# Performance work log

Measured on AMD Instinct MI355X. Metric: run time of the kernel, lower is better.

## Reference

```python
import jax, jax.numpy as jnp
import numpy as np

INPUT_SIZE = 768
HIDDEN = 512


def _lstm_dir(x_tbi, h0, c0, w_ih, w_hh, b_ih, b_hh):
    """Single-direction LSTM over time-major input. Returns all hidden states [T,B,H].
    PyTorch gate order: i, f, g, o."""
    # Precompute input contribution for all timesteps (one big GEMM).
    gx = jnp.einsum('tbi,gi->tbg', x_tbi, w_ih) + (b_ih + b_hh)  # [T,B,4H]

    def step(carry, gx_t):
        h, c = carry
        gates = gx_t + h @ w_hh.T  # [B,4H]
        i, f, g, o = jnp.split(gates, 4, axis=-1)
        i = jax.nn.sigmoid(i)
        f = jax.nn.sigmoid(f)
        g = jnp.tanh(g)
        o = jax.nn.sigmoid(o)
        c = f * c + i * g
        h = o * jnp.tanh(c)
        return (h, c), h

    (_, _), hs = jax.lax.scan(step, (h0, c0), gx)
    return hs  # [T,B,H]


def setup_inputs() -> dict:
    key = jax.random.key(0)
    ks = jax.random.split(key, 12)
    B, T = 32, 512
    scale = 1.0 / np.sqrt(HIDDEN)

    def unif(k, shape):
        return jax.random.uniform(k, shape, jnp.float32, -scale, scale)

    return {
        'x': jax.random.normal(ks[0], (B, T, INPUT_SIZE), jnp.float32),
        'h0': jax.random.normal(ks[1], (2, B, HIDDEN), jnp.float32),
        'c0': jax.random.normal(ks[2], (2, B, HIDDEN), jnp.float32),
        'w_ih_f': unif(ks[3], (4 * HIDDEN, INPUT_SIZE)),
        'w_hh_f': unif(ks[4], (4 * HIDDEN, HIDDEN)),
        'b_ih_f': unif(ks[5], (4 * HIDDEN,)),
        'b_hh_f': unif(ks[6], (4 * HIDDEN,)),
        'w_ih_b': unif(ks[7], (4 * HIDDEN, INPUT_SIZE)),
        'w_hh_b': unif(ks[8], (4 * HIDDEN, HIDDEN)),
        'b_ih_b': unif(ks[9], (4 * HIDDEN,)),
        'b_hh_b': unif(ks[10], (4 * HIDDEN,)),
    }


def reference(x, h0, c0, w_ih_f, w_hh_f, b_ih_f, b_hh_f,
              w_ih_b, w_hh_b, b_ih_b, b_hh_b):
    # x: [B,T,I] (batch_first) -> time-major [T,B,I]
    x_tbi = jnp.transpose(x, (1, 0, 2))
    hs_f = _lstm_dir(x_tbi, h0[0], c0[0], w_ih_f, w_hh_f, b_ih_f, b_hh_f)
    hs_b = _lstm_dir(x_tbi[::-1], h0[1], c0[1], w_ih_b, w_hh_b, b_ih_b, b_hh_b)
    # out[:, -1, :]: forward dir at last step = hs_f[-1];
    # backward dir at last time index = first scan step over reversed seq = hs_b[0]
    last = jnp.concatenate([hs_f[-1], hs_b[0]], axis=-1)  # [B, 2H]
    return jax.nn.relu(last)
```

## Files before the change

kernel.cpp:

```cpp
#include <hip/hip_runtime.h>


typedef __attribute__((ext_vector_type(4))) float         floatx4;
typedef __attribute__((ext_vector_type(4))) unsigned int  uintx4;
typedef __attribute__((ext_vector_type(8))) unsigned short ushortx8;
typedef __attribute__((ext_vector_type(4))) unsigned short ushortx4;
typedef __attribute__((ext_vector_type(8))) __bf16        bf16x8;

#define NBLK 32
#define GRID_TOTAL 256
#define DONE_MAGIC 0xDEADBEEFu

__device__ __forceinline__ unsigned short f2bf(float f) {
  unsigned u = __builtin_bit_cast(unsigned, f);
  return (unsigned short)((u + 0x7fffu + ((u >> 16) & 1u)) >> 16);
}
__device__ __forceinline__ float bf2f(unsigned short h) {
  unsigned u = ((unsigned)h) << 16;
  return __builtin_bit_cast(float, u);
}
__device__ __forceinline__ floatx4 mfma_bf16(ushortx8 a, ushortx8 b, floatx4 c) {
  return __builtin_amdgcn_mfma_f32_16x16x32_bf16(
      __builtin_bit_cast(bf16x8, a), __builtin_bit_cast(bf16x8, b), c, 0, 0, 0);
}
__device__ __forceinline__ float sigmoidf_(float x) { return 1.f / (1.f + __expf(-x)); }
__device__ __forceinline__ float tanhf_(float x) {
  float ax = fabsf(x);
  float e = __expf(-2.f * ax);
  float r = (1.f - e) / (1.f + e);
  return x < 0.f ? -r : r;
}

__global__ void cvt_w_kernel(const float* __restrict__ src, unsigned short* __restrict__ dst, int n) {
  int i = (blockIdx.x * 256 + threadIdx.x) * 4;
  if (i < n) {
    floatx4 v = *reinterpret_cast<const floatx4*>(src + i);
    ushortx4 o;
    o[0] = f2bf(v[0]); o[1] = f2bf(v[1]); o[2] = f2bf(v[2]); o[3] = f2bf(v[3]);
    *reinterpret_cast<ushortx4*>(dst + i) = o;
  }
}

__global__ __launch_bounds__(256) void gx_kernel(
    const float* __restrict__ x, const unsigned short* __restrict__ w_bf,
    const float* __restrict__ b_ih, const float* __restrict__ b_hh,
    unsigned short* __restrict__ gxbuf) {
  const int t = blockIdx.y;
  const int nb = blockIdx.x;
  const int tid = threadIdx.x;
  const int wave = tid >> 6;
  const int lane = tid & 63;
  const int l15 = lane & 15;
  const int lq = lane >> 4;

  __shared__ __align__(16) unsigned short x_lds[32][776];

  {
    const int row = tid >> 3, c8 = tid & 7;
    const floatx4* src = reinterpret_cast<const floatx4*>(x + ((size_t)row * 512 + t) * 768);
#pragma unroll
    for (int m = 0; m < 24; ++m) {
      int col4 = c8 + m * 8;
      floatx4 v = src[col4];
      ushortx4 o;
      o[0] = f2bf(v[0]); o[1] = f2bf(v[1]); o[2] = f2bf(v[2]); o[3] = f2bf(v[3]);
      *reinterpret_cast<ushortx4*>(&x_lds[row][col4 * 4]) = o;
    }
  }
  __syncthreads();

  const int wgs = nb * 4;
  const ushortx8* brow[4];
#pragma unroll
  for (int nt = 0; nt < 4; ++nt) {
    int n = wave * 512 + (wgs + nt) * 16 + l15;
    brow[nt] = reinterpret_cast<const ushortx8*>(w_bf + (size_t)n * 768);
  }

  floatx4 acc[4][2];
#pragma unroll
  for (int nt = 0; nt < 4; ++nt) { acc[nt][0] = (floatx4)0.f; acc[nt][1] = (floatx4)0.f; }

  for (int q = 0; q < 24; ++q) {
    ushortx8 a0 = *reinterpret_cast<const ushortx8*>(&x_lds[l15][q * 32 + lq * 8]);
    ushortx8 a1 = *reinterpret_cast<const ushortx8*>(&x_lds[16 + l15][q * 32 + lq * 8]);
#pragma unroll
    for (int nt = 0; nt < 4; ++nt) {
      ushortx8 bf = brow[nt][q * 4 + lq];
      acc[nt][0] = mfma_bf16(a0, bf, acc[nt][0]);
      acc[nt][1] = mfma_bf16(a1, bf, acc[nt][1]);
    }
  }

#pragma unroll
  for (int nt = 0; nt < 4; ++nt) {
    int wg = wgs + nt;
    int N = wave * 512 + wg * 16 + l15;
    float bias = b_ih[N] + b_hh[N];
    unsigned short* dst = gxbuf + ((size_t)(t * 32 + wg)) * 2048 + wave * 512 + l15;
#pragma unroll
    for (int m = 0; m < 2; ++m)
#pragma unroll
      for (int r = 0; r < 4; ++r) {
        int b = m * 16 + lq * 4 + r;
        dst[b * 16] = f2bf(acc[nt][m][r] + bias);
      }
  }
}

__global__ __launch_bounds__(256) void bwd_kernel(
    const float* __restrict__ x, const float* __restrict__ h0, const float* __restrict__ c0,
    const float* __restrict__ w_ih_b, const float* __restrict__ w_hh_b,
    const float* __restrict__ b_ih_b, const float* __restrict__ b_hh_b,
    float* __restrict__ out) {
  const int wg = blockIdx.x;
  const int tid = threadIdx.x;
  const int wave = tid >> 6;
  const int lane = tid & 63;
  const int l15 = lane & 15;
  const int lq = lane >> 4;

  __shared__ __align__(16) unsigned short cat_lds[32][1288];
  __shared__ __align__(16) float gate_lds[4][32][16];

  {
    const int row = tid >> 3, o8 = tid & 7;
    const floatx4* xs = reinterpret_cast<const floatx4*>(x + ((size_t)row * 512 + 511) * 768);
#pragma unroll
    for (int m = 0; m < 24; ++m) {
      int col4 = o8 + m * 8;
      floatx4 v = xs[col4];
      ushortx4 o;
      o[0] = f2bf(v[0]); o[1] = f2bf(v[1]); o[2] = f2bf(v[2]); o[3] = f2bf(v[3]);
      *reinterpret_cast<ushortx4*>(&cat_lds[row][col4 * 4]) = o;
    }
    const floatx4* hs = reinterpret_cast<const floatx4*>(h0 + (size_t)(32 + row) * 512);
#pragma unroll
    for (int m = 0; m < 16; ++m) {
      int col4 = o8 + m * 8;
      floatx4 v = hs[col4];
      ushortx4 o;
      o[0] = f2bf(v[0]); o[1] = f2bf(v[1]); o[2] = f2bf(v[2]); o[3] = f2bf(v[3]);
      *reinterpret_cast<ushortx4*>(&cat_lds[row][768 + col4 * 4]) = o;
    }
  }
  __syncthreads();

  const int n = wave * 512 + wg * 16 + l15;
  floatx4 acc0 = (floatx4)0.f, acc1 = (floatx4)0.f;
  for (int q = 0; q < 40; ++q) {
    int k0 = q * 32;
    const float* wsrc = (k0 < 768) ? (w_ih_b + (size_t)n * 768 + k0 + lq * 8)
                                   : (w_hh_b + (size_t)n * 512 + (k0 - 768) + lq * 8);
    ushortx8 bf;
#pragma unroll
    for (int j = 0; j < 8; ++j) bf[j] = f2bf(wsrc[j]);
    ushortx8 a0 = *reinterpret_cast<const ushortx8*>(&cat_lds[l15][k0 + lq * 8]);
    ushortx8 a1 = *reinterpret_cast<const ushortx8*>(&cat_lds[16 + l15][k0 + lq * 8]);
    acc0 = mfma_bf16(a0, bf, acc0);
    acc1 = mfma_bf16(a1, bf, acc1);
  }
#pragma unroll
  for (int r = 0; r < 4; ++r) {
    gate_lds[wave][lq * 4 + r][l15] = acc0[r];
    gate_lds[wave][16 + lq * 4 + r][l15] = acc1[r];
  }
  __syncthreads();

  {
    const int jj = tid & 15;
    const int b0 = tid >> 4;
    const int col = wg * 16 + jj;
    float bi[4];
#pragma unroll
    for (int g = 0; g < 4; ++g) bi[g] = b_ih_b[g * 512 + col] + b_hh_b[g * 512 + col];
#pragma unroll
    for (int half = 0; half < 2; ++half) {
      int b = b0 + half * 16;
      float gi = sigmoidf_(gate_lds[0][b][jj] + bi[0]);
      float gf = sigmoidf_(gate_lds[1][b][jj] + bi[1]);
      float gg = tanhf_(gate_lds[2][b][jj] + bi[2]);
      float go = sigmoidf_(gate_lds[3][b][jj] + bi[3]);
      float c = gf * c0[(size_t)(32 + b) * 512 + col] + gi * gg;
      float h = go * tanhf_(c);
      out[(size_t)b * 1024 + 512 + col] = fmaxf(h, 0.f);
    }
  }
}

__global__ __launch_bounds__(256, 1) void lstm_fwd_kernel(
    const float* __restrict__ w_hh, const unsigned short* __restrict__ gxbuf,
    const float* __restrict__ h0, const float* __restrict__ c0,
    unsigned long long* gbuf64, unsigned* flags, float* sink,
    float* __restrict__ out) {
  const int tid = threadIdx.x;

  if ((blockIdx.x & 7) != 0) {
    __shared__ unsigned sdone;
    float a0 = 1.0f + 1e-7f * (float)(tid + 1);
    float a1 = 1.0f - 1e-7f * (float)(tid + 2);
    float a2 = 1.0f + 2e-7f * (float)(tid + 3);
    float a3 = 1.0f - 2e-7f * (float)(tid + 4);
    const float m0 = 0.99999994f;
    unsigned d;
    do {
#pragma unroll 8
      for (int i = 0; i < 2048; ++i) {
        a0 = fmaf(a0, m0, 1e-7f);
        a1 = fmaf(a1, m0, -1e-7f);
        a2 = fmaf(a2, m0, 2e-7f);
        a3 = fmaf(a3, m0, -2e-7f);
      }
      if (tid == 0)
        sdone = __hip_atomic_load(&flags[0], __ATOMIC_RELAXED, __HIP_MEMORY_SCOPE_AGENT);
      __syncthreads();
      d = sdone;
      __syncthreads();
    } while (d != DONE_MAGIC);
    if (a0 + a1 + a2 + a3 == 3.14159f) sink[blockIdx.x] = a0;
    return;
  }

  const int wg = blockIdx.x >> 3;
  const int wave = tid >> 6;
  const int lane = tid & 63;
  const int l15 = lane & 15;
  const int lq = lane >> 4;

  __shared__ __align__(16) unsigned short h_lds[32][520];
  __shared__ __align__(16) float gate_lds[4][32][16];
  __shared__ __align__(16) unsigned short gx_lds[2][2048];

  ushortx8 wfrag[16];
  {
    const int n = wave * 512 + wg * 16 + l15;
    const float* wrow = w_hh + (size_t)n * 512 + lq * 8;
#pragma unroll
    for (int q = 0; q < 16; ++q) {
      ushortx8 f;
#pragma unroll
      for (int j = 0; j < 8; ++j) f[j] = f2bf(wrow[q * 32 + j]);
      wfrag[q] = f;
    }
  }

  const int b_ = tid >> 3;
  const int j0 = (tid & 7) * 2;
  const int col0 = wg * 16 + j0;
  float c_0 = c0[(size_t)b_ * 512 + col0];
  float c_1 = c0[(size_t)b_ * 512 + col0 + 1];

  {
    unsigned data = (unsigned)f2bf(h0[(size_t)b_ * 512 + col0]) |
                    ((unsigned)f2bf(h0[(size_t)b_ * 512 + col0 + 1]) << 16);
    unsigned long long w = ((unsigned long long)data << 32) | 1ull;
    __hip_atomic_store(&gbuf64[b_ * 256 + (col0 >> 1)], w, __ATOMIC_RELAXED, __HIP_MEMORY_SCOPE_AGENT);
  }

  const uintx4* gxp = reinterpret_cast<const uintx4*>(gxbuf);
  uintx4 gxreg = gxp[(size_t)(0 * 32 + wg) * 256 + tid];

#pragma unroll 1
  for (int t = 0; t < 512; ++t) {
    *reinterpret_cast<uintx4*>(&gx_lds[t & 1][tid * 8]) = gxreg;
    if (t + 1 < 512) gxreg = gxp[(size_t)((t + 1) * 32 + wg) * 256 + tid];

    {
      unsigned long long* src = gbuf64 + (size_t)(t & 1) * 8192;
      const unsigned target = (unsigned)(t + 1);
      unsigned long long w[32];
      bool ok;
      do {
#pragma unroll
        for (int k = 0; k < 32; ++k)
          w[k] = __hip_atomic_load(&src[tid + k * 256], __ATOMIC_RELAXED, __HIP_MEMORY_SCOPE_AGENT);
        ok = true;
#pragma unroll
        for (int k = 0; k < 32; ++k) ok &= ((unsigned)w[k] == target);
      } while (!ok);
#pragma unroll
      for (int k = 0; k < 32; ++k)
        *reinterpret_cast<unsigned*>(&h_lds[k][tid * 2]) = (unsigned)(w[k] >> 32);
    }
    __syncthreads();

    floatx4 acc0 = (floatx4)0.f, acc1 = (floatx4)0.f;
#pragma unroll
    for (int q = 0; q < 16; ++q) {
      ushortx8 a0 = *reinterpret_cast<const ushortx8*>(&h_lds[l15][q * 32 + lq * 8]);
      ushortx8 a1 = *reinterpret_cast<const ushortx8*>(&h_lds[16 + l15][q * 32 + lq * 8]);
      acc0 = mfma_bf16(a0, wfrag[q], acc0);
      acc1 = mfma_bf16(a1, wfrag[q], acc1);
    }
#pragma unroll
    for (int r = 0; r < 4; ++r) {
      gate_lds[wave][lq * 4 + r][l15] = acc0[r];
      gate_lds[wave][16 + lq * 4 + r][l15] = acc1[r];
    }
    __syncthreads();

    {
      const unsigned short* gx = gx_lds[t & 1];
      float i0 = sigmoidf_(gate_lds[0][b_][j0] + bf2f(gx[(0 * 32 + b_) * 16 + j0]));
      float f0 = sigmoidf_(gate_lds[1][b_][j0] + bf2f(gx[(1 * 32 + b_) * 16 + j0]));
      float g0 = tanhf_(gate_lds[2][b_][j0] + bf2f(gx[(2 * 32 + b_) * 16 + j0]));
      float o0 = sigmoidf_(gate_lds[3][b_][j0] + bf2f(gx[(3 * 32 + b_) * 16 + j0]));
      c_0 = f0 * c_0 + i0 * g0;
      float ha = o0 * tanhf_(c_0);

      float i1 = sigmoidf_(gate_lds[0][b_][j0 + 1] + bf2f(gx[(0 * 32 + b_) * 16 + j0 + 1]));
      float f1 = sigmoidf_(gate_lds[1][b_][j0 + 1] + bf2f(gx[(1 * 32 + b_) * 16 + j0 + 1]));
      float g1 = tanhf_(gate_lds[2][b_][j0 + 1] + bf2f(gx[(2 * 32 + b_) * 16 + j0 + 1]));
      float o1 = sigmoidf_(gate_lds[3][b_][j0 + 1] + bf2f(gx[(3 * 32 + b_) * 16 + j0 + 1]));
      c_1 = f1 * c_1 + i1 * g1;
      float hb = o1 * tanhf_(c_1);

      unsigned data = (unsigned)f2bf(ha) | ((unsigned)f2bf(hb) << 16);
      unsigned long long w = ((unsigned long long)data << 32) | (unsigned long long)(t + 2);
      unsigned long long* hdst = gbuf64 + (size_t)((t + 1) & 1) * 8192;
      __hip_atomic_store(&hdst[b_ * 256 + (col0 >> 1)], w, __ATOMIC_RELAXED, __HIP_MEMORY_SCOPE_AGENT);
      if (t == 511) {
        out[(size_t)b_ * 1024 + col0] = fmaxf(ha, 0.f);
        out[(size_t)b_ * 1024 + col0 + 1] = fmaxf(hb, 0.f);
      }
    }
  }

  if (wg == 0 && tid == 0)
    __hip_atomic_store(&flags[0], DONE_MAGIC, __ATOMIC_RELAXED, __HIP_MEMORY_SCOPE_AGENT);
}

extern "C" void kernel_launch(void* const* d_in, const int* in_sizes, int n_in,
                              void* d_out, int out_size, void* d_ws, size_t ws_size,
                              hipStream_t stream) {
  const float* x      = (const float*)d_in[0];
  const float* h0     = (const float*)d_in[1];
  const float* c0     = (const float*)d_in[2];
  const float* w_ih_f = (const float*)d_in[3];
  const float* w_hh_f = (const float*)d_in[4];
  const float* b_ih_f = (const float*)d_in[5];
  const float* b_hh_f = (const float*)d_in[6];
  const float* w_ih_b = (const float*)d_in[7];
  const float* w_hh_b = (const float*)d_in[8];
  const float* b_ih_b = (const float*)d_in[9];
  const float* b_hh_b = (const float*)d_in[10];
  float* out = (float*)d_out;

  char* ws = (char*)d_ws;
  unsigned short* gxbuf      = (unsigned short*)(ws);
  unsigned short* wihbf      = (unsigned short*)(ws + (size_t)67108864);
  unsigned long long* gbuf64 = (unsigned long long*)(ws + (size_t)67108864 + 3145728);
  unsigned* flags            = (unsigned*)(ws + (size_t)67108864 + 3145728 + 131072);
  float* sink                = (float*)(ws + (size_t)67108864 + 3145728 + 131072 + 1024);

  hipMemsetAsync(flags, 0, 256, stream);
  hipLaunchKernelGGL(cvt_w_kernel, dim3(1536), dim3(256), 0, stream, w_ih_f, wihbf, 1572864);
  hipLaunchKernelGGL(gx_kernel, dim3(8, 512), dim3(256), 0, stream, x, wihbf, b_ih_f, b_hh_f, gxbuf);
  hipLaunchKernelGGL(bwd_kernel, dim3(32), dim3(256), 0, stream, x, h0, c0,
                     w_ih_b, w_hh_b, b_ih_b, b_hh_b, out);
  hipLaunchKernelGGL(lstm_fwd_kernel, dim3(GRID_TOTAL), dim3(256), 0, stream,
                     w_hh_f, gxbuf, h0, c0, gbuf64, flags, sink, out);
}
```

Before: 1.884 ms.

## Split recurrent LSTM batch into two independent 16-row groups with separate mailboxes

The forward recurrent kernel now uses two block groups per hidden slice (g=0,1), each owning 16 of the 32 batch rows and exchanging h through its own mailbox region. Each block polls half as much state and issues one MFMA chain per step instead of two, so the per-step critical path should shrink. The spin-wait idle blocks now wait for a completion counter of 2 instead of a magic value. In exchange, twice as many blocks take part in the grid-wide spin synchronization, and half the threads sit idle in the elementwise phase.

```diff
diff --git a/kernel.cpp b/kernel.cpp
--- a/kernel.cpp
+++ b/kernel.cpp
@@ -7,9 +7,8 @@
 typedef __attribute__((ext_vector_type(4))) unsigned short ushortx4;
 typedef __attribute__((ext_vector_type(8))) __bf16        bf16x8;
 
-#define NBLK 32
 #define GRID_TOTAL 256
-#define DONE_MAGIC 0xDEADBEEFu
+#define DONE_COUNT 2u
 
 __device__ __forceinline__ unsigned short f2bf(float f) {
   unsigned u = __builtin_bit_cast(unsigned, f);
@@ -194,8 +193,9 @@
     unsigned long long* gbuf64, unsigned* flags, float* sink,
     float* __restrict__ out) {
   const int tid = threadIdx.x;
-
-  if ((blockIdx.x & 7) != 0) {
+  const int g = blockIdx.x & 7;
+
+  if (g >= 2) {
     __shared__ unsigned sdone;
     float a0 = 1.0f + 1e-7f * (float)(tid + 1);
     float a1 = 1.0f - 1e-7f * (float)(tid + 2);
@@ -216,7 +216,7 @@
       __syncthreads();
       d = sdone;
       __syncthreads();
-    } while (d != DONE_MAGIC);
+    } while (d < DONE_COUNT);
     if (a0 + a1 + a2 + a3 == 3.14159f) sink[blockIdx.x] = a0;
     return;
   }
@@ -227,9 +227,9 @@
   const int l15 = lane & 15;
   const int lq = lane >> 4;
 
-  __shared__ __align__(16) unsigned short h_lds[32][520];
-  __shared__ __align__(16) float gate_lds[4][32][16];
-  __shared__ __align__(16) unsigned short gx_lds[2][2048];
+  __shared__ __align__(16) unsigned short h_lds[16][520];
+  __shared__ __align__(16) float gate_lds[4][16][16];
+  __shared__ __align__(16) unsigned short gx_lds[2][1024];
 
   ushortx8 wfrag[16];
   {
@@ -244,90 +244,95 @@
     }
   }
 
-  const int b_ = tid >> 3;
-  const int j0 = (tid & 7) * 2;
+  unsigned long long* mbox = gbuf64 + (size_t)g * 8192;
+
+  const int r_ = tid >> 3;
+  const int jp = tid & 7;
+  const int j0 = jp * 2;
   const int col0 = wg * 16 + j0;
-  float c_0 = c0[(size_t)b_ * 512 + col0];
-  float c_1 = c0[(size_t)b_ * 512 + col0 + 1];
-
-  {
-    unsigned data = (unsigned)f2bf(h0[(size_t)b_ * 512 + col0]) |
-                    ((unsigned)f2bf(h0[(size_t)b_ * 512 + col0 + 1]) << 16);
-    unsigned long long w = ((unsigned long long)data << 32) | 1ull;
-    __hip_atomic_store(&gbuf64[b_ * 256 + (col0 >> 1)], w, __ATOMIC_RELAXED, __HIP_MEMORY_SCOPE_AGENT);
-  }
-
-  const uintx4* gxp = reinterpret_cast<const uintx4*>(gxbuf);
-  uintx4 gxreg = gxp[(size_t)(0 * 32 + wg) * 256 + tid];
+  const int grow = g * 16 + r_;
+  float c_0 = 0.f, c_1 = 0.f;
+  if (r_ < 16) {
+    c_0 = c0[(size_t)grow * 512 + col0];
+    c_1 = c0[(size_t)grow * 512 + col0 + 1];
+    unsigned data = (unsigned)f2bf(h0[(size_t)grow * 512 + col0]) |
+                    ((unsigned)f2bf(h0[(size_t)grow * 512 + col0 + 1]) << 16);
+    unsigned long long wd = ((unsigned long long)data << 32) | 1ull;
+    __hip_atomic_store(&mbox[r_ * 256 + (col0 >> 1)], wd, __ATOMIC_RELAXED, __HIP_MEMORY_SCOPE_AGENT);
+  }
+
+  const unsigned long long* gxq = reinterpret_cast<const unsigned long long*>(gxbuf);
+  const int gxoff = wave * 128 + g * 64 + (tid & 63);
+  unsigned long long gxreg = gxq[(size_t)(0 * 32 + wg) * 512 + gxoff];
 
 #pragma unroll 1
   for (int t = 0; t < 512; ++t) {
-    *reinterpret_cast<uintx4*>(&gx_lds[t & 1][tid * 8]) = gxreg;
-    if (t + 1 < 512) gxreg = gxp[(size_t)((t + 1) * 32 + wg) * 256 + tid];
+    reinterpret_cast<unsigned long long*>(gx_lds[t & 1])[tid] = gxreg;
+    if (t + 1 < 512) gxreg = gxq[(size_t)((t + 1) * 32 + wg) * 512 + gxoff];
 
     {
-      unsigned long long* src = gbuf64 + (size_t)(t & 1) * 8192;
+      unsigned long long* src = mbox + (size_t)(t & 1) * 4096;
       const unsigned target = (unsigned)(t + 1);
-      unsigned long long w[32];
+      unsigned long long wv[16];
       bool ok;
       do {
 #pragma unroll
-        for (int k = 0; k < 32; ++k)
-          w[k] = __hip_atomic_load(&src[tid + k * 256], __ATOMIC_RELAXED, __HIP_MEMORY_SCOPE_AGENT);
+        for (int k = 0; k < 16; ++k)
+          wv[k] = __hip_atomic_load(&src[tid + k * 256], __ATOMIC_RELAXED, __HIP_MEMORY_SCOPE_AGENT);
         ok = true;
 #pragma unroll
-        for (int k = 0; k < 32; ++k) ok &= ((unsigned)w[k] == target);
+        for (int k = 0; k < 16; ++k) ok &= ((unsigned)wv[k] == target);
       } while (!ok);
 #pragma unroll
-      for (int k = 0; k < 32; ++k)
-        *reinterpret_cast<unsigned*>(&h_lds[k][tid * 2]) = (unsigned)(w[k] >> 32);
+      for (int k = 0; k < 16; ++k) {
+        int f = tid + k * 256;
+        *reinterpret_cast<unsigned*>(&h_lds[f >> 8][(f & 255) * 2]) = (unsigned)(wv[k] >> 32);
+      }
     }
     __syncthreads();
 
-    floatx4 acc0 = (floatx4)0.f, acc1 = (floatx4)0.f;
+    floatx4 acc = (floatx4)0.f;
 #pragma unroll
     for (int q = 0; q < 16; ++q) {
-      ushortx8 a0 = *reinterpret_cast<const ushortx8*>(&h_lds[l15][q * 32 + lq * 8]);
-      ushortx8 a1 = *reinterpret_cast<const ushortx8*>(&h_lds[16 + l15][q * 32 + lq * 8]);
-      acc0 = mfma_bf16(a0, wfrag[q], acc0);
-      acc1 = mfma_bf16(a1, wfrag[q], acc1);
-    }
-#pragma unroll
-    for (int r = 0; r < 4; ++r) {
-      gate_lds[wave][lq * 4 + r][l15] = acc0[r];
-      gate_lds[wave][16 + lq * 4 + r][l15] = acc1[r];
-    }
+      ushortx8 a = *reinterpret_cast<const ushortx8*>(&h_lds[l15][q * 32 + lq * 8]);
+      acc = mfma_bf16(a, wfrag[q], acc);
+    }
+#pragma unroll
+    for (int r = 0; r < 4; ++r)
+      gate_lds[wave][lq * 4 + r][l15] = acc[r];
     __syncthreads();
 
-    {
+    if (r_ < 16) {
       const unsigned short* gx = gx_lds[t & 1];
-      float i0 = sigmoidf_(gate_lds[0][b_][j0] + bf2f(gx[(0 * 32 + b_) * 16 + j0]));
-      float f0 = sigmoidf_(gate_lds[1][b_][j0] + bf2f(gx[(1 * 32 + b_) * 16 + j0]));
-      float g0 = tanhf_(gate_lds[2][b_][j0] + bf2f(gx[(2 * 32 + b_) * 16 + j0]));
-      float o0 = sigmoidf_(gate_lds[3][b_][j0] + bf2f(gx[(3 * 32 + b_) * 16 + j0]));
+      float p0 = gate_lds[0][r_][j0] + bf2f(gx[0 * 256 + r_ * 16 + j0]);
+      float p1 = gate_lds[1][r_][j0] + bf2f(gx[1 * 256 + r_ * 16 + j0]);
+      float p2 = gate_lds[2][r_][j0] + bf2f(gx[2 * 256 + r_ * 16 + j0]);
+      float p3 = gate_lds[3][r_][j0] + bf2f(gx[3 * 256 + r_ * 16 + j0]);
+      float i0 = sigmoidf_(p0), f0 = sigmoidf_(p1), g0 = tanhf_(p2), o0 = sigmoidf_(p3);
       c_0 = f0 * c_0 + i0 * g0;
       float ha = o0 * tanhf_(c_0);
 
-      float i1 = sigmoidf_(gate_lds[0][b_][j0 + 1] + bf2f(gx[(0 * 32 + b_) * 16 + j0 + 1]));
-      float f1 = sigmoidf_(gate_lds[1][b_][j0 + 1] + bf2f(gx[(1 * 32 + b_) * 16 + j0 + 1]));
-      float g1 = tanhf_(gate_lds[2][b_][j0 + 1] + bf2f(gx[(2 * 32 + b_) * 16 + j0 + 1]));
-      float o1 = sigmoidf_(gate_lds[3][b_][j0 + 1] + bf2f(gx[(3 * 32 + b_) * 16 + j0 + 1]));
+      float q0 = gate_lds[0][r_][j0 + 1] + bf2f(gx[0 * 256 + r_ * 16 + j0 + 1]);
+      float q1 = gate_lds[1][r_][j0 + 1] + bf2f(gx[1 * 256 + r_ * 16 + j0 + 1]);
+      float q2 = gate_lds[2][r_][j0 + 1] + bf2f(gx[2 * 256 + r_ * 16 + j0 + 1]);
+      float q3 = gate_lds[3][r_][j0 + 1] + bf2f(gx[3 * 256 + r_ * 16 + j0 + 1]);
+      float i1 = sigmoidf_(q0), f1 = sigmoidf_(q1), g1 = tanhf_(q2), o1 = sigmoidf_(q3);
       c_1 = f1 * c_1 + i1 * g1;
       float hb = o1 * tanhf_(c_1);
 
       unsigned data = (unsigned)f2bf(ha) | ((unsigned)f2bf(hb) << 16);
-      unsigned long long w = ((unsigned long long)data << 32) | (unsigned long long)(t + 2);
-      unsigned long long* hdst = gbuf64 + (size_t)((t + 1) & 1) * 8192;
-      __hip_atomic_store(&hdst[b_ * 256 + (col0 >> 1)], w, __ATOMIC_RELAXED, __HIP_MEMORY_SCOPE_AGENT);
+      unsigned long long wd = ((unsigned long long)data << 32) | (unsigned long long)(t + 2);
+      unsigned long long* hdst = mbox + (size_t)((t + 1) & 1) * 4096;
+      __hip_atomic_store(&hdst[r_ * 256 + (col0 >> 1)], wd, __ATOMIC_RELAXED, __HIP_MEMORY_SCOPE_AGENT);
       if (t == 511) {
-        out[(size_t)b_ * 1024 + col0] = fmaxf(ha, 0.f);
-        out[(size_t)b_ * 1024 + col0 + 1] = fmaxf(hb, 0.f);
+        out[(size_t)grow * 1024 + col0] = fmaxf(ha, 0.f);
+        out[(size_t)grow * 1024 + col0 + 1] = fmaxf(hb, 0.f);
       }
     }
   }
 
   if (wg == 0 && tid == 0)
-    __hip_atomic_store(&flags[0], DONE_MAGIC, __ATOMIC_RELAXED, __HIP_MEMORY_SCOPE_AGENT);
+    __hip_atomic_fetch_add(&flags[0], 1u, __ATOMIC_RELAXED, __HIP_MEMORY_SCOPE_AGENT);
 }
 
 extern "C" void kernel_launch(void* const* d_in, const int* in_sizes, int n_in,
```

Result: slower. 2.091 ms (+11.0%).
